# Kernel tuning notes

Hardware: AMD Instinct MI355X
Metric: run time of the kernel (lower is better)

Reference implementation:

```python
import jax, jax.numpy as jnp
import numpy as np

EPS = 1e-05
NEG = -1000000000.0

def rmsnorm(x):
    var = jnp.mean(x * x, axis=-1, keepdims=True)
    return x * jax.lax.rsqrt(var + EPS)

def apply_rotary(x, cos, sin):
    # x: [B,T,H,D], cos/sin: [T,D]
    d = x.shape[-1]
    x1, x2 = x[..., : d // 2], x[..., d // 2 :]
    half_rot = jnp.concatenate([-x2, x1], axis=-1)
    c = cos[None, :, None, :]
    s = sin[None, :, None, :]
    return x * c + half_rot * s

def setup_inputs() -> dict:
    key = jax.random.key(0)
    ks = jax.random.split(key, 12)
    B, T, C, H = 2, 2048, 1024, 16
    hd = C // H
    std = 0.02
    return {
        "x": jax.random.normal(ks[0], (B, T, C), jnp.float32),
        "x0": jax.random.normal(ks[1], (B, T, C), jnp.float32),
        "lambdaResid": jnp.ones((), jnp.float32),
        "lambdaX0": jnp.ones((), jnp.float32),
        "cos": jax.random.uniform(ks[2], (T, hd), jnp.float32),
        "sin": jax.random.uniform(ks[3], (T, hd), jnp.float32),
        "qWeight": jax.random.normal(ks[4], (C, C), jnp.float32) * std,
        "kWeight": jax.random.normal(ks[5], (C, C), jnp.float32) * std,
        "vWeight": jax.random.normal(ks[6], (C, C), jnp.float32) * std,
        "projWeight": jax.random.normal(ks[7], (C, C), jnp.float32) * std,
        "fcWeight": jax.random.normal(ks[8], (C, 4 * C), jnp.float32) * std,
        "mlpProjWeight": jax.random.normal(ks[9], (4 * C, C), jnp.float32) * std,
    }

def reference(x, x0, lambdaResid, lambdaX0, cos, sin,
              qWeight, kWeight, vWeight, projWeight, fcWeight, mlpProjWeight):
    B, T, C = x.shape
    hd = cos.shape[-1]
    H = C // hd
    scaled = x * lambdaResid + x0 * lambdaX0
    pre = rmsnorm(scaled)
    q = (pre @ qWeight).reshape(B, T, H, hd)
    k = (pre @ kWeight).reshape(B, T, H, hd)
    v = (pre @ vWeight).reshape(B, T, H, hd)
    q = rmsnorm(apply_rotary(q, cos, sin))  # [B,T,H,D]
    k = rmsnorm(apply_rotary(k, cos, sin))
    scores = jnp.einsum('bthd,bshd->bhts', q, k) / jnp.sqrt(jnp.float32(hd))
    mask = jnp.tril(jnp.ones((T, T), bool))
    scores = jnp.where(mask[None, None], scores, NEG)
    probs = jax.nn.softmax(scores, axis=-1)
    attn = jnp.einsum('bhts,bshd->bthd', probs, v).reshape(B, T, C)
    scaled = scaled + attn @ projWeight
    h = rmsnorm(scaled) @ fcWeight
    h = jnp.square(jax.nn.relu(h))
    return scaled + h @ mlpProjWeight
```

## Files before the change

kernel.cpp:

```cpp
#include <hip/hip_runtime.h>
#include <hip/hip_bf16.h>
#include <stdint.h>

typedef _Float16 f16;
typedef __attribute__((ext_vector_type(8))) _Float16 f16x8;
typedef __attribute__((ext_vector_type(4))) _Float16 f16x4;
typedef __attribute__((ext_vector_type(4))) float f32x4;

__device__ __forceinline__ void g2l16(const void* g, void* l) {
  __builtin_amdgcn_global_load_lds(
      (const __attribute__((address_space(1))) uint32_t*)g,
      (__attribute__((address_space(3))) uint32_t*)l, 16, 0, 0);
}

__global__ __launch_bounds__(256)
void wconv_all_kernel(const float* __restrict__ Wq, const float* __restrict__ Wk,
                      const float* __restrict__ Wv, const float* __restrict__ Wp,
                      const float* __restrict__ Wfc, const float* __restrict__ Wmp,
                      f16* __restrict__ Dq, f16* __restrict__ Dk, f16* __restrict__ Dv,
                      f16* __restrict__ Dp, f16* __restrict__ Dfc, f16* __restrict__ Dmp)
{
  __shared__ float tile[32][33];
  int id = blockIdx.x;
  const float* W; f16* Wt; int K, N, local;
  if      (id < 1024) { W = Wq;  Wt = Dq;  K = 1024; N = 1024; local = id; }
  else if (id < 2048) { W = Wk;  Wt = Dk;  K = 1024; N = 1024; local = id - 1024; }
  else if (id < 3072) { W = Wv;  Wt = Dv;  K = 1024; N = 1024; local = id - 2048; }
  else if (id < 4096) { W = Wp;  Wt = Dp;  K = 1024; N = 1024; local = id - 3072; }
  else if (id < 8192) { W = Wfc; Wt = Dfc; K = 1024; N = 4096; local = id - 4096; }
  else                { W = Wmp; Wt = Dmp; K = 4096; N = 1024; local = id - 8192; }
  int ntx = N >> 5;
  int n0 = (local % ntx) * 32, k0 = (local / ntx) * 32;
  int tx = threadIdx.x & 31, ty = threadIdx.x >> 5;
#pragma unroll
  for (int i = 0; i < 4; ++i)
    tile[ty + 8*i][tx] = W[(size_t)(k0 + ty + 8*i) * N + (n0 + tx)];
  __syncthreads();
#pragma unroll
  for (int i = 0; i < 4; ++i)
    Wt[(size_t)(n0 + ty + 8*i) * K + (k0 + tx)] = (f16)tile[tx][ty + 8*i];
}

__global__ __launch_bounds__(256)
void scale_rms_kernel(const float* __restrict__ x, const float* __restrict__ x0,
                      const float* __restrict__ lamR, const float* __restrict__ lamX,
                      float* __restrict__ scaled, f16* __restrict__ pre)
{
  const int C = 1024;
  int row = blockIdx.x, tid = threadIdx.x;
  float lr = lamR[0], lx = lamX[0];
  size_t base = (size_t)row * C;
  float4 xv = ((const float4*)(x + base))[tid];
  float4 zv = ((const float4*)(x0 + base))[tid];
  float4 sv;
  sv.x = xv.x*lr + zv.x*lx;  sv.y = xv.y*lr + zv.y*lx;
  sv.z = xv.z*lr + zv.z*lx;  sv.w = xv.w*lr + zv.w*lx;
  float ss = sv.x*sv.x + sv.y*sv.y + sv.z*sv.z + sv.w*sv.w;
#pragma unroll
  for (int off = 32; off >= 1; off >>= 1) ss += __shfl_xor(ss, off);
  __shared__ float red[4];
  if ((tid & 63) == 0) red[tid >> 6] = ss;
  __syncthreads();
  float tot = red[0] + red[1] + red[2] + red[3];
  float rs = rsqrtf(tot * (1.0f / 1024.0f) + 1e-5f);
  ((float4*)(scaled + base))[tid] = sv;
  f16* p = pre + base + tid * 4;
  p[0] = (f16)(sv.x * rs); p[1] = (f16)(sv.y * rs);
  p[2] = (f16)(sv.z * rs); p[3] = (f16)(sv.w * rs);
}

__global__ __launch_bounds__(256)
void combine_rms_kernel(const float* __restrict__ resid, const f16* __restrict__ p0,
                        const f16* __restrict__ p1, float* __restrict__ scaled2,
                        f16* __restrict__ pre2)
{
  const int C = 1024;
  int row = blockIdx.x, tid = threadIdx.x;
  size_t base = (size_t)row * C;
  float4 rv = ((const float4*)(resid + base))[tid];
  f16x4 av = ((const f16x4*)(p0 + base))[tid];
  f16x4 bv = ((const f16x4*)(p1 + base))[tid];
  float4 sv;
  sv.x = rv.x + (float)av[0] + (float)bv[0];
  sv.y = rv.y + (float)av[1] + (float)bv[1];
  sv.z = rv.z + (float)av[2] + (float)bv[2];
  sv.w = rv.w + (float)av[3] + (float)bv[3];
  float ss = sv.x*sv.x + sv.y*sv.y + sv.z*sv.z + sv.w*sv.w;
#pragma unroll
  for (int off = 32; off >= 1; off >>= 1) ss += __shfl_xor(ss, off);
  __shared__ float red[4];
  if ((tid & 63) == 0) red[tid >> 6] = ss;
  __syncthreads();
  float tot = red[0] + red[1] + red[2] + red[3];
  float rs = rsqrtf(tot * (1.0f / 1024.0f) + 1e-5f);
  ((float4*)(scaled2 + base))[tid] = sv;
  f16* p = pre2 + base + tid * 4;
  p[0] = (f16)(sv.x * rs); p[1] = (f16)(sv.y * rs);
  p[2] = (f16)(sv.z * rs); p[3] = (f16)(sv.w * rs);
}

__global__ __launch_bounds__(256)
void combine_out4_kernel(const float* __restrict__ resid, const f16* __restrict__ parts,
                         size_t pstride, float* __restrict__ out)
{
  size_t i = (size_t)blockIdx.x * 256 + threadIdx.x;
  float4 rv = ((const float4*)resid)[i];
  float4 sv = rv;
#pragma unroll
  for (int z = 0; z < 4; ++z) {
    f16x4 av = ((const f16x4*)(parts + z * pstride))[i];
    sv.x += (float)av[0]; sv.y += (float)av[1];
    sv.z += (float)av[2]; sv.w += (float)av[3];
  }
  ((float4*)out)[i] = sv;
}

__global__ __launch_bounds__(256)
void rope_rms_kernel(f16* __restrict__ Xq, f16* __restrict__ Xk,
                     const float* __restrict__ cs, const float* __restrict__ sn)
{
  const int MH = 4096 * 16;
  int ridx = blockIdx.x * 4 + (threadIdx.x >> 6);
  f16* X = (ridx < MH) ? Xq : Xk;
  if (ridx >= MH) ridx -= MH;
  int lane = threadIdx.x & 63;
  int h = ridx & 15;
  int bt = ridx >> 4;
  int t = bt & 2047;
  size_t base = (size_t)bt * 1024 + h * 64;
  float xv = (float)X[base + lane];
  float other = __shfl_xor(xv, 32);
  float rot = (lane < 32) ? -other : other;
  float c = cs[t * 64 + lane], s = sn[t * 64 + lane];
  float y = xv * c + rot * s;
  float ss = y * y;
#pragma unroll
  for (int off = 32; off >= 1; off >>= 1) ss += __shfl_xor(ss, off);
  float r = rsqrtf(ss * (1.0f / 64.0f) + 1e-5f);
  X[base + lane] = (f16)(y * r);
}

template<int EPI>
__global__ __launch_bounds__(256)
void gemm_kernel(const f16* __restrict__ A, const f16* __restrict__ Bt,
                 void* __restrict__ out, int M, int N, int K, int nb, int zb)
{
  __shared__ __align__(16) f16 smem[4 * 128 * 32];
  const int tid = threadIdx.x;
  const int wave = tid >> 6, lane = tid & 63;
  const int col = lane & 15, quad = lane >> 4;
  const int id = blockIdx.x;
  const int xcd = id & 7, s = id >> 3;
  const int n_i = s % nb;
  const int p = s / nb;
  const int mpx = (M >> 7) >> 3;
  const int zz = p / mpx;
  const int m_i = xcd * mpx + (p % mpx);
  const int m0 = m_i * 128, n0 = n_i * 128;
  const int wm = (wave >> 1) * 64, wn = (wave & 1) * 64;
  const int Ksub = K / zb;
  const int kBeg = zz * Ksub;
  const int nIter = Ksub >> 5;
  f32x4 acc[4][4] = {};

  const size_t rowb = (size_t)K * 2;
  const char* Agp = (const char*)A  + (size_t)m0 * rowb;
  const char* Bgp = (const char*)Bt + (size_t)n0 * rowb;

  const int r_st = (tid >> 2);
  const int cb_st = (tid & 3) << 4;
  const int lb0 = (wave * 64) << 4;
  const int lb1 = (256 + wave * 64) << 4;

#define STAGE(buf, k0)                                                           \
  {                                                                              \
    const size_t koff = (size_t)(k0) * 2;                                        \
    g2l16(Agp + (size_t)r_st * rowb + koff + cb_st,                              \
          (char*)smem + (buf) * 8192 + lb0);                                     \
    g2l16(Agp + (size_t)(r_st + 64) * rowb + koff + cb_st,                       \
          (char*)smem + (buf) * 8192 + lb1);                                     \
    g2l16(Bgp + (size_t)r_st * rowb + koff + cb_st,                              \
          (char*)smem + 16384 + (buf) * 8192 + lb0);                             \
    g2l16(Bgp + (size_t)(r_st + 64) * rowb + koff + cb_st,                       \
          (char*)smem + 16384 + (buf) * 8192 + lb1);                             \
  }

  STAGE(0, kBeg)
  for (int kt = 0; kt < nIter; ++kt) {
    __syncthreads();
    if (kt + 1 < nIter) STAGE((kt + 1) & 1, kBeg + (kt + 1) * 32)
    const f16* As = smem + (kt & 1) * 4096;
    const f16* Bs = smem + 8192 + (kt & 1) * 4096;
    f16x8 af[4], bf[4];
#pragma unroll
    for (int t = 0; t < 4; ++t)
      af[t] = *(const f16x8*)(As + (wm + t*16 + col) * 32 + quad * 8);
#pragma unroll
    for (int t = 0; t < 4; ++t)
      bf[t] = *(const f16x8*)(Bs + (wn + t*16 + col) * 32 + quad * 8);
#pragma unroll
    for (int mt = 0; mt < 4; ++mt)
#pragma unroll
      for (int nt = 0; nt < 4; ++nt)
        acc[mt][nt] = __builtin_amdgcn_mfma_f32_16x16x32_f16(af[mt], bf[nt], acc[mt][nt], 0, 0, 0);
  }
#undef STAGE
  f16* ep = smem + wave * 1024;
  f16* outz = (EPI == 4) ? ((f16*)out + (size_t)zz * M * N) : (f16*)out;
#pragma unroll
  for (int mt = 0; mt < 4; ++mt) {
#pragma unroll
    for (int nt = 0; nt < 4; ++nt) {
#pragma unroll
      for (int r = 0; r < 4; ++r) {
        float v = acc[mt][nt][r];
        if (EPI == 1) { float tv = v > 0.0f ? v : 0.0f; v = tv * tv; }
        ep[(quad * 4 + r) * 64 + ((nt ^ quad) * 16 + col)] = (f16)v;
      }
    }
#pragma unroll
    for (int j = 0; j < 2; ++j) {
      int e = j * 64 + lane;
      int row = e >> 3, rb = e & 7;
      int phys16 = (((rb >> 1) ^ (row >> 2)) << 1) + (rb & 1);
      f16x8 vv = *(const f16x8*)(ep + row * 64 + phys16 * 8);
      int grow = m0 + wm + mt * 16 + row;
      int gcol = n0 + wn + rb * 8;
      *(f16x8*)(outz + (size_t)grow * N + gcol) = vv;
    }
  }
}


__device__ __forceinline__ void stage256(const char* Agp, const char* Bgp, size_t rowb,
                                         char* lds, int st_r, size_t koff, int tid)
{
#pragma unroll
  for (int j = 0; j < 4; ++j) {
    g2l16(Agp + (size_t)(st_r + j * 64) * rowb + koff, lds + j * 8192 + tid * 16);
    g2l16(Bgp + (size_t)(st_r + j * 64) * rowb + koff, lds + 32768 + j * 8192 + tid * 16);
  }
}

template<int EPI>
__global__ __launch_bounds__(512, 2)
void gemm256_kernel(const f16* __restrict__ A, const f16* __restrict__ Bt,
                    void* __restrict__ out, int M, int N, int K, int nb, int zb)
{
  __shared__ __align__(16) f16 smem[65536];
  const int tid = threadIdx.x;
  const int wave = tid >> 6, lane = tid & 63;
  const int col = lane & 15, quad = lane >> 4;
  const int id = blockIdx.x;
  const int xcd = id & 7, sb = id >> 3;
  const int n_i = sb % nb;
  const int p = sb / nb;
  const int mpx = (M >> 8) >> 3;
  const int zz = p / mpx;
  const int m_i = xcd * mpx + (p % mpx);
  const int m0 = m_i * 256, n0 = n_i * 256;
  const int wm = (wave >> 2) * 128, wn = (wave & 3) * 64;
  const int Ksub = K / zb;
  const int kBeg = zz * Ksub;
  const int ntiles = Ksub >> 6;
  f32x4 acc[8][4] = {};

  const size_t rowb = (size_t)K * 2;
  const char* Agp = (const char*)A  + (size_t)m0 * rowb;
  const char* Bgp = (const char*)Bt + (size_t)n0 * rowb;

  const int st_r = tid >> 3;
  const size_t st_so = (size_t)(((tid & 7) ^ ((tid >> 3) & 7)) << 4);

  stage256(Agp, Bgp, rowb, (char*)smem,         st_r, (size_t)kBeg * 2 + st_so, tid);
  stage256(Agp, Bgp, rowb, (char*)smem + 65536, st_r, (size_t)(kBeg + 64) * 2 + st_so, tid);

  for (int t = 0; t < ntiles; ++t) {
    if (t < ntiles - 1) asm volatile("s_waitcnt vmcnt(8)" ::: "memory");
    else                asm volatile("s_waitcnt vmcnt(0)" ::: "memory");
    __builtin_amdgcn_s_barrier();
    asm volatile("" ::: "memory");

    const f16* As = smem + (t & 1) * 32768;
    const f16* Bs = As + 16384;
    f16x8 bf[4][2];
#pragma unroll
    for (int ct = 0; ct < 4; ++ct)
#pragma unroll
      for (int ks = 0; ks < 2; ++ks)
        bf[ct][ks] = *(const f16x8*)(Bs + (wn + ct*16 + col) * 64 +
                                     (((ks*4 + quad) ^ (col & 7)) << 3));
#pragma unroll
    for (int sp = 0; sp < 4; ++sp) {
      f16x8 af[2][2];
#pragma unroll
      for (int i = 0; i < 2; ++i)
#pragma unroll
        for (int ks = 0; ks < 2; ++ks)
          af[i][ks] = *(const f16x8*)(As + (wm + (sp*2 + i)*16 + col) * 64 +
                                      (((ks*4 + quad) ^ (col & 7)) << 3));
      __builtin_amdgcn_s_setprio(1);
#pragma unroll
      for (int i = 0; i < 2; ++i)
#pragma unroll
        for (int ct = 0; ct < 4; ++ct)
#pragma unroll
          for (int ks = 0; ks < 2; ++ks)
            acc[sp*2 + i][ct] = __builtin_amdgcn_mfma_f32_16x16x32_f16(
                af[i][ks], bf[ct][ks], acc[sp*2 + i][ct], 0, 0, 0);
      __builtin_amdgcn_s_setprio(0);
    }

    asm volatile("s_waitcnt lgkmcnt(0)" ::: "memory");
    __builtin_amdgcn_s_barrier();
    asm volatile("" ::: "memory");
    if (t + 2 < ntiles)
      stage256(Agp, Bgp, rowb, (char*)smem + (t & 1) * 65536, st_r,
               (size_t)(kBeg + (t + 2) * 64) * 2 + st_so, tid);
  }

  f16* ep = smem + wave * 1024;
  f16* outz = (EPI == 4) ? ((f16*)out + (size_t)zz * M * N) : (f16*)out;
#pragma unroll
  for (int mt = 0; mt < 8; ++mt) {
#pragma unroll
    for (int ct = 0; ct < 4; ++ct) {
#pragma unroll
      for (int r = 0; r < 4; ++r) {
        float v = acc[mt][ct][r];
        if (EPI == 1) { float tv = v > 0.0f ? v : 0.0f; v = tv * tv; }
        ep[(quad * 4 + r) * 64 + ((ct ^ quad) * 16 + col)] = (f16)v;
      }
    }
#pragma unroll
    for (int j = 0; j < 2; ++j) {
      int e = j * 64 + lane;
      int row = e >> 3, rb = e & 7;
      int phys16 = (((rb >> 1) ^ (row >> 2)) << 1) + (rb & 1);
      f16x8 vv = *(const f16x8*)(ep + row * 64 + phys16 * 8);
      int grow = m0 + wm + mt * 16 + row;
      int gcol = n0 + wn + rb * 8;
      *(f16x8*)(outz + (size_t)grow * N + gcol) = vv;
    }
  }
}

__global__ __launch_bounds__(512, 2)
void gemm256_qkv_kernel(const f16* __restrict__ A, const f16* __restrict__ Bt,
                        f16* __restrict__ qb, f16* __restrict__ kbuf, f16* __restrict__ vtg)
{
  const int K = 1024, nb = 12, ntiles = 16;
  __shared__ __align__(16) f16 smem[65536];
  const int tid = threadIdx.x;
  const int wave = tid >> 6, lane = tid & 63;
  const int col = lane & 15, quad = lane >> 4;
  const int id = blockIdx.x;
  const int xcd = id & 7, sb = id >> 3;
  const int n_i = sb % nb;
  const int m_i = xcd * 2 + (sb / nb);
  const int m0 = m_i * 256, n0 = n_i * 256;
  const int wm = (wave >> 2) * 128, wn = (wave & 3) * 64;
  f32x4 acc[8][4] = {};

  const size_t rowb = (size_t)K * 2;
  const char* Agp = (const char*)A  + (size_t)m0 * rowb;
  const char* Bgp = (const char*)Bt + (size_t)n0 * rowb;

  const int st_r = tid >> 3;
  const size_t st_so = (size_t)(((tid & 7) ^ ((tid >> 3) & 7)) << 4);

  stage256(Agp, Bgp, rowb, (char*)smem,         st_r, st_so, tid);
  stage256(Agp, Bgp, rowb, (char*)smem + 65536, st_r, (size_t)64 * 2 + st_so, tid);

  for (int t = 0; t < ntiles; ++t) {
    if (t < ntiles - 1) asm volatile("s_waitcnt vmcnt(8)" ::: "memory");
    else                asm volatile("s_waitcnt vmcnt(0)" ::: "memory");
    __builtin_amdgcn_s_barrier();
    asm volatile("" ::: "memory");

    const f16* As = smem + (t & 1) * 32768;
    const f16* Bs = As + 16384;
    f16x8 bf[4][2];
#pragma unroll
    for (int ct = 0; ct < 4; ++ct)
#pragma unroll
      for (int ks = 0; ks < 2; ++ks)
        bf[ct][ks] = *(const f16x8*)(Bs + (wn + ct*16 + col) * 64 +
                                     (((ks*4 + quad) ^ (col & 7)) << 3));
#pragma unroll
    for (int sp = 0; sp < 4; ++sp) {
      f16x8 af[2][2];
#pragma unroll
      for (int i = 0; i < 2; ++i)
#pragma unroll
        for (int ks = 0; ks < 2; ++ks)
          af[i][ks] = *(const f16x8*)(As + (wm + (sp*2 + i)*16 + col) * 64 +
                                      (((ks*4 + quad) ^ (col & 7)) << 3));
      __builtin_amdgcn_s_setprio(1);
#pragma unroll
      for (int i = 0; i < 2; ++i)
#pragma unroll
        for (int ct = 0; ct < 4; ++ct)
#pragma unroll
          for (int ks = 0; ks < 2; ++ks)
            acc[sp*2 + i][ct] = __builtin_amdgcn_mfma_f32_16x16x32_f16(
                af[i][ks], bf[ct][ks], acc[sp*2 + i][ct], 0, 0, 0);
      __builtin_amdgcn_s_setprio(0);
    }

    asm volatile("s_waitcnt lgkmcnt(0)" ::: "memory");
    __builtin_amdgcn_s_barrier();
    asm volatile("" ::: "memory");
    if (t + 2 < ntiles)
      stage256(Agp, Bgp, rowb, (char*)smem + (t & 1) * 65536, st_r,
               (size_t)((t + 2) * 64) * 2 + st_so, tid);
  }

  const int cw = n0 + wn;
  const int sel = cw >> 10;
  if (sel < 2) {
    f16* dst = (sel == 0) ? qb : kbuf;
    const int cbase = cw & 1023;
    f16* ep = smem + wave * 1024;
#pragma unroll
    for (int mt = 0; mt < 8; ++mt) {
#pragma unroll
      for (int ct = 0; ct < 4; ++ct)
#pragma unroll
        for (int r = 0; r < 4; ++r)
          ep[(quad * 4 + r) * 64 + ((ct ^ quad) * 16 + col)] = (f16)acc[mt][ct][r];
#pragma unroll
      for (int j = 0; j < 2; ++j) {
        int e = j * 64 + lane;
        int row = e >> 3, rb = e & 7;
        int phys16 = (((rb >> 1) ^ (row >> 2)) << 1) + (rb & 1);
        f16x8 vv = *(const f16x8*)(ep + row * 64 + phys16 * 8);
        int grow = m0 + wm + mt * 16 + row;
        *(f16x8*)(dst + (size_t)grow * 1024 + cbase + rb * 8) = vv;
      }
    }
  } else {
#pragma unroll
    for (int mt = 0; mt < 8; ++mt) {
      int t0 = m0 + wm + mt * 16 + quad * 4;
      int b = t0 >> 11, t = t0 & 2047;
#pragma unroll
      for (int ct = 0; ct < 4; ++ct) {
        int dd = (cw & 1023) + ct * 16 + col;
        int hh = dd >> 6, d = dd & 63;
        f16x4 vv;
#pragma unroll
        for (int r = 0; r < 4; ++r) vv[r] = (f16)acc[mt][ct][r];
        *(f16x4*)(vtg + ((size_t)((b * 16 + hh) * 64 + d)) * 2048 + t) = vv;
      }
    }
  }
}

__global__ __launch_bounds__(256)
void attn_kernel(const f16* __restrict__ Q, const f16* __restrict__ Kc,
                 const f16* __restrict__ Vt, f16* __restrict__ O)
{
  const int T = 2048, C = 1024;
  __shared__ __align__(16) f16 Ks[2][64 * 64];
  __shared__ __align__(16) f16 Vs[2][64 * 64];
  __shared__ __align__(16) f16 Ps[4][16 * 64];
  const int tid = threadIdx.x, wave = tid >> 6, lane = tid & 63;
  const int col = lane & 15, quad = lane >> 4;
  const int bh = blockIdx.x, b = bh >> 4, h = bh & 15;
  const int qt = (int)gridDim.y - 1 - (int)blockIdx.y;
  const int q0 = qt * 64;

  const f16* qb = Q  + ((size_t)b * T) * C + h * 64;
  const f16* kb = Kc + ((size_t)b * T) * C + h * 64;
  const f16* vb = Vt + ((size_t)bh * 64) * T;

  f16x8 aq[2];
#pragma unroll
  for (int ks = 0; ks < 2; ++ks)
    aq[ks] = *(const f16x8*)(qb + (size_t)(q0 + wave*16 + col) * C + ks*32 + quad*8);

  f32x4 o_acc[4];
#pragma unroll
  for (int dt = 0; dt < 4; ++dt) o_acc[dt] = (f32x4){0.f,0.f,0.f,0.f};
  float l_part[4] = {0.f, 0.f, 0.f, 0.f};

  const int srow = lane >> 3;
  const int sblk = (lane & 7) ^ srow;

#pragma unroll
  for (int i = 0; i < 2; ++i) {
    int r0 = wave * 16 + 8 * i;
    g2l16(kb + (size_t)(r0 + srow) * C + sblk * 8, (char*)Ks[0] + r0 * 128);
    g2l16(vb + (size_t)(r0 + srow) * T + sblk * 8, (char*)Vs[0] + r0 * 128);
  }

  int cur = 0;
  for (int kt = 0; kt <= qt; ++kt) {
    __syncthreads();

    if (kt < qt) {
      const int ks1 = (kt + 1) * 64;
#pragma unroll
      for (int i = 0; i < 2; ++i) {
        int r0 = wave * 16 + 8 * i;
        g2l16(kb + (size_t)(ks1 + r0 + srow) * C + sblk * 8, (char*)Ks[cur ^ 1] + r0 * 128);
        g2l16(vb + (size_t)(r0 + srow) * T + ks1 + sblk * 8, (char*)Vs[cur ^ 1] + r0 * 128);
      }
    }

    f32x4 s[4];
#pragma unroll
    for (int nt = 0; nt < 4; ++nt) s[nt] = (f32x4){0.f,0.f,0.f,0.f};
#pragma unroll
    for (int ks = 0; ks < 2; ++ks) {
#pragma unroll
      for (int nt = 0; nt < 4; ++nt) {
        int key = nt * 16 + col;
        f16x8 bk = *(const f16x8*)(Ks[cur] + key * 64 + (((ks*4 + quad) ^ (key & 7)) * 8));
        s[nt] = __builtin_amdgcn_mfma_f32_16x16x32_f16(aq[ks], bk, s[nt], 0, 0, 0);
      }
    }

    const bool masked = (kt == qt);
#pragma unroll
    for (int r = 0; r < 4; ++r) {
      const int qloc = quad * 4 + r;
      float p[4];
#pragma unroll
      for (int nt = 0; nt < 4; ++nt) {
        float pv = __expf(s[nt][r] * 0.125f);
        if (masked && (nt * 16 + col > wave * 16 + qloc)) pv = 0.0f;
        p[nt] = pv;
      }
      l_part[r] += (p[0] + p[1]) + (p[2] + p[3]);
#pragma unroll
      for (int nt = 0; nt < 4; ++nt) {
        int kblk = nt * 2 + (col >> 3);
        Ps[wave][qloc * 64 + ((kblk ^ (qloc & 7)) * 8) + (col & 7)] = (f16)p[nt];
      }
    }

#pragma unroll
    for (int ks = 0; ks < 2; ++ks) {
      f16x8 ap = *(const f16x8*)(&Ps[wave][0] + col * 64 + (((ks*4 + quad) ^ (col & 7)) * 8));
#pragma unroll
      for (int dt = 0; dt < 4; ++dt) {
        int d = dt * 16 + col;
        f16x8 bv = *(const f16x8*)(Vs[cur] + d * 64 + (((ks*4 + quad) ^ (d & 7)) * 8));
        o_acc[dt] = __builtin_amdgcn_mfma_f32_16x16x32_f16(ap, bv, o_acc[dt], 0, 0, 0);
      }
    }
    cur ^= 1;
  }

#pragma unroll
  for (int r = 0; r < 4; ++r) {
#pragma unroll
    for (int off = 8; off >= 1; off >>= 1)
      l_part[r] += __shfl_xor(l_part[r], off, 16);
  }
#pragma unroll
  for (int dt = 0; dt < 4; ++dt) {
#pragma unroll
    for (int r = 0; r < 4; ++r) {
      int qr = q0 + wave * 16 + quad * 4 + r;
      float v = o_acc[dt][r] / l_part[r];
      O[((size_t)b * T + qr) * C + h * 64 + dt * 16 + col] = (f16)v;
    }
  }
}

extern "C" void kernel_launch(void* const* d_in, const int* in_sizes, int n_in,
                              void* d_out, int out_size, void* d_ws, size_t ws_size,
                              hipStream_t stream)
{
  const float* x    = (const float*)d_in[0];
  const float* x0   = (const float*)d_in[1];
  const float* lamR = (const float*)d_in[2];
  const float* lamX = (const float*)d_in[3];
  const float* cs   = (const float*)d_in[4];
  const float* sn   = (const float*)d_in[5];
  const float* Wq   = (const float*)d_in[6];
  const float* Wk   = (const float*)d_in[7];
  const float* Wv   = (const float*)d_in[8];
  const float* Wp   = (const float*)d_in[9];
  const float* Wfc  = (const float*)d_in[10];
  const float* Wmp  = (const float*)d_in[11];
  float* out = (float*)d_out;

  const int B = 2, T = 2048, C = 1024, H = 16;
  const int M = B * T;
  const size_t MB = 1ull << 20;
  char* ws = (char*)d_ws;
  f16*   Wqkv_t = (f16*)(ws + 0 * MB);
  f16*   Wp_t   = (f16*)(ws + 6 * MB);
  f16*   Wfc_t  = (f16*)(ws + 8 * MB);
  f16*   Wmp_t  = (f16*)(ws + 16 * MB);
  float* scaled  = (float*)(ws + 24 * MB);
  f16*   pre     = (f16*)(ws + 40 * MB);
  f16*   qb      = (f16*)(ws + 48 * MB);
  f16*   kbuf    = (f16*)(ws + 56 * MB);
  f16*   vtg     = (f16*)(ws + 64 * MB);
  float* scaled2 = (float*)(ws + 72 * MB);
  f16*   hbuf    = (f16*)(ws + 88 * MB);
  f16*   attnOut = pre;
  f16*   pre2    = qb;
  f16*   projP   = (f16*)(ws + 88 * MB);
  f16*   mlpP    = (f16*)(ws + 24 * MB);

  dim3 tb(256);
  dim3 tb5(512);
  wconv_all_kernel<<<dim3(12288), tb, 0, stream>>>(
      Wq, Wk, Wv, Wp, Wfc, Wmp,
      Wqkv_t, Wqkv_t + 1024*1024, Wqkv_t + 2048*1024, Wp_t, Wfc_t, Wmp_t);

  scale_rms_kernel<<<M, tb, 0, stream>>>(x, x0, lamR, lamX, scaled, pre);

  gemm256_qkv_kernel<<<dim3(192), tb5, 0, stream>>>(pre, Wqkv_t, qb, kbuf, vtg);

  rope_rms_kernel<<<(M * H) / 2, tb, 0, stream>>>(qb, kbuf, cs, sn);

  attn_kernel<<<dim3(B * H, T/64), tb, 0, stream>>>(qb, kbuf, vtg, attnOut);

  gemm_kernel<4><<<dim3(8 * 32 * 2), tb, 0, stream>>>(attnOut, Wp_t, projP, M, C, C, 8, 2);
  combine_rms_kernel<<<M, tb, 0, stream>>>(scaled, projP, projP + (size_t)M*C, scaled2, pre2);

  gemm256_kernel<1><<<dim3(256), tb5, 0, stream>>>(pre2, Wfc_t, hbuf, M, 4*C, C, 16, 1);

  gemm256_kernel<4><<<dim3(256), tb5, 0, stream>>>(hbuf, Wmp_t, mlpP, M, C, 4*C, 4, 4);
  combine_out4_kernel<<<(M*C)/1024, tb, 0, stream>>>(scaled2, mlpP, (size_t)M*C, out);
}
```

Baseline: 349.8 us.

## Pair causal query tiles per attention block to balance work and share K/V loads

The attention kernel now launches 512-thread blocks, each handling two query tiles: a high tile (31-pr) with one four-wave group and a low tile (pr) with the other. The two groups share the double-buffered K/V tiles in LDS, so each key tile is loaded once for both. Pairing tiles this way gives every block the same amount of causal work and halves the grid. The low-tile waves go idle once they pass their diagonal but still hit the barriers, and the larger block may reduce occupancy.

New measurement: 347.6 us. No clear change (-0.6%).

```diff
diff --git a/kernel.cpp b/kernel.cpp
--- a/kernel.cpp
+++ b/kernel.cpp
@@ -231,7 +231,6 @@
   }
 }
 
-
 __device__ __forceinline__ void stage256(const char* Agp, const char* Bgp, size_t rowb,
                                          char* lds, int st_r, size_t koff, int tid)
 {
@@ -457,19 +456,23 @@
   }
 }
 
-__global__ __launch_bounds__(256)
+__global__ __launch_bounds__(512)
 void attn_kernel(const f16* __restrict__ Q, const f16* __restrict__ Kc,
                  const f16* __restrict__ Vt, f16* __restrict__ O)
 {
   const int T = 2048, C = 1024;
   __shared__ __align__(16) f16 Ks[2][64 * 64];
   __shared__ __align__(16) f16 Vs[2][64 * 64];
-  __shared__ __align__(16) f16 Ps[4][16 * 64];
+  __shared__ __align__(16) f16 Ps[8][16 * 64];
   const int tid = threadIdx.x, wave = tid >> 6, lane = tid & 63;
   const int col = lane & 15, quad = lane >> 4;
   const int bh = blockIdx.x, b = bh >> 4, h = bh & 15;
-  const int qt = (int)gridDim.y - 1 - (int)blockIdx.y;
-  const int q0 = qt * 64;
+  const int pr = blockIdx.y;
+  const int grp = wave >> 2;
+  const int w4 = wave & 3;
+  const int hiB = 31 - pr;
+  const int myB = grp ? pr : hiB;
+  const int q0 = myB * 64;
 
   const f16* qb = Q  + ((size_t)b * T) * C + h * 64;
   const f16* kb = Kc + ((size_t)b * T) * C + h * 64;
@@ -478,7 +481,7 @@
   f16x8 aq[2];
 #pragma unroll
   for (int ks = 0; ks < 2; ++ks)
-    aq[ks] = *(const f16x8*)(qb + (size_t)(q0 + wave*16 + col) * C + ks*32 + quad*8);
+    aq[ks] = *(const f16x8*)(qb + (size_t)(q0 + w4*16 + col) * C + ks*32 + quad*8);
 
   f32x4 o_acc[4];
 #pragma unroll
@@ -487,68 +490,63 @@
 
   const int srow = lane >> 3;
   const int sblk = (lane & 7) ^ srow;
-
-#pragma unroll
-  for (int i = 0; i < 2; ++i) {
-    int r0 = wave * 16 + 8 * i;
-    g2l16(kb + (size_t)(r0 + srow) * C + sblk * 8, (char*)Ks[0] + r0 * 128);
-    g2l16(vb + (size_t)(r0 + srow) * T + sblk * 8, (char*)Vs[0] + r0 * 128);
-  }
+  const int r0 = wave * 8;
+
+  g2l16(kb + (size_t)(r0 + srow) * C + sblk * 8, (char*)Ks[0] + r0 * 128);
+  g2l16(vb + (size_t)(r0 + srow) * T + sblk * 8, (char*)Vs[0] + r0 * 128);
 
   int cur = 0;
-  for (int kt = 0; kt <= qt; ++kt) {
+  for (int kt = 0; kt <= hiB; ++kt) {
     __syncthreads();
 
-    if (kt < qt) {
+    if (kt < hiB) {
       const int ks1 = (kt + 1) * 64;
-#pragma unroll
-      for (int i = 0; i < 2; ++i) {
-        int r0 = wave * 16 + 8 * i;
-        g2l16(kb + (size_t)(ks1 + r0 + srow) * C + sblk * 8, (char*)Ks[cur ^ 1] + r0 * 128);
-        g2l16(vb + (size_t)(r0 + srow) * T + ks1 + sblk * 8, (char*)Vs[cur ^ 1] + r0 * 128);
+      g2l16(kb + (size_t)(ks1 + r0 + srow) * C + sblk * 8, (char*)Ks[cur ^ 1] + r0 * 128);
+      g2l16(vb + (size_t)(r0 + srow) * T + ks1 + sblk * 8, (char*)Vs[cur ^ 1] + r0 * 128);
+    }
+
+    if (kt <= myB) {
+      f32x4 s[4];
+#pragma unroll
+      for (int nt = 0; nt < 4; ++nt) s[nt] = (f32x4){0.f,0.f,0.f,0.f};
+#pragma unroll
+      for (int ks = 0; ks < 2; ++ks) {
+#pragma unroll
+        for (int nt = 0; nt < 4; ++nt) {
+          int key = nt * 16 + col;
+          f16x8 bk = *(const f16x8*)(Ks[cur] + key * 64 + (((ks*4 + quad) ^ (key & 7)) * 8));
+          s[nt] = __builtin_amdgcn_mfma_f32_16x16x32_f16(aq[ks], bk, s[nt], 0, 0, 0);
+        }
       }
-    }
-
-    f32x4 s[4];
-#pragma unroll
-    for (int nt = 0; nt < 4; ++nt) s[nt] = (f32x4){0.f,0.f,0.f,0.f};
-#pragma unroll
-    for (int ks = 0; ks < 2; ++ks) {
-#pragma unroll
-      for (int nt = 0; nt < 4; ++nt) {
-        int key = nt * 16 + col;
-        f16x8 bk = *(const f16x8*)(Ks[cur] + key * 64 + (((ks*4 + quad) ^ (key & 7)) * 8));
-        s[nt] = __builtin_amdgcn_mfma_f32_16x16x32_f16(aq[ks], bk, s[nt], 0, 0, 0);
+
+      const bool masked = (kt == myB);
+#pragma unroll
+      for (int r = 0; r < 4; ++r) {
+        const int qloc = quad * 4 + r;
+        float p[4];
+#pragma unroll
+        for (int nt = 0; nt < 4; ++nt) {
+          float pv = __expf(s[nt][r] * 0.125f);
+          if (masked && (nt * 16 + col > w4 * 16 + qloc)) pv = 0.0f;
+          p[nt] = pv;
+        }
+        l_part[r] += (p[0] + p[1]) + (p[2] + p[3]);
+#pragma unroll
+        for (int nt = 0; nt < 4; ++nt) {
+          int kblk = nt * 2 + (col >> 3);
+          Ps[wave][qloc * 64 + ((kblk ^ (qloc & 7)) * 8) + (col & 7)] = (f16)p[nt];
+        }
       }
-    }
-
-    const bool masked = (kt == qt);
-#pragma unroll
-    for (int r = 0; r < 4; ++r) {
-      const int qloc = quad * 4 + r;
-      float p[4];
-#pragma unroll
-      for (int nt = 0; nt < 4; ++nt) {
-        float pv = __expf(s[nt][r] * 0.125f);
-        if (masked && (nt * 16 + col > wave * 16 + qloc)) pv = 0.0f;
-        p[nt] = pv;
-      }
-      l_part[r] += (p[0] + p[1]) + (p[2] + p[3]);
-#pragma unroll
-      for (int nt = 0; nt < 4; ++nt) {
-        int kblk = nt * 2 + (col >> 3);
-        Ps[wave][qloc * 64 + ((kblk ^ (qloc & 7)) * 8) + (col & 7)] = (f16)p[nt];
-      }
-    }
-
-#pragma unroll
-    for (int ks = 0; ks < 2; ++ks) {
-      f16x8 ap = *(const f16x8*)(&Ps[wave][0] + col * 64 + (((ks*4 + quad) ^ (col & 7)) * 8));
-#pragma unroll
-      for (int dt = 0; dt < 4; ++dt) {
-        int d = dt * 16 + col;
-        f16x8 bv = *(const f16x8*)(Vs[cur] + d * 64 + (((ks*4 + quad) ^ (d & 7)) * 8));
-        o_acc[dt] = __builtin_amdgcn_mfma_f32_16x16x32_f16(ap, bv, o_acc[dt], 0, 0, 0);
+
+#pragma unroll
+      for (int ks = 0; ks < 2; ++ks) {
+        f16x8 ap = *(const f16x8*)(&Ps[wave][0] + col * 64 + (((ks*4 + quad) ^ (col & 7)) * 8));
+#pragma unroll
+        for (int dt = 0; dt < 4; ++dt) {
+          int d = dt * 16 + col;
+          f16x8 bv = *(const f16x8*)(Vs[cur] + d * 64 + (((ks*4 + quad) ^ (d & 7)) * 8));
+          o_acc[dt] = __builtin_amdgcn_mfma_f32_16x16x32_f16(ap, bv, o_acc[dt], 0, 0, 0);
+        }
       }
     }
     cur ^= 1;
@@ -564,7 +562,7 @@
   for (int dt = 0; dt < 4; ++dt) {
 #pragma unroll
     for (int r = 0; r < 4; ++r) {
-      int qr = q0 + wave * 16 + quad * 4 + r;
+      int qr = q0 + w4 * 16 + quad * 4 + r;
       float v = o_acc[dt][r] / l_part[r];
       O[((size_t)b * T + qr) * C + h * 64 + dt * 16 + col] = (f16)v;
     }
@@ -621,7 +619,7 @@
 
   rope_rms_kernel<<<(M * H) / 2, tb, 0, stream>>>(qb, kbuf, cs, sn);
 
-  attn_kernel<<<dim3(B * H, T/64), tb, 0, stream>>>(qb, kbuf, vtg, attnOut);
+  attn_kernel<<<dim3(B * H, 16), tb5, 0, stream>>>(qb, kbuf, vtg, attnOut);
 
   gemm_kernel<4><<<dim3(8 * 32 * 2), tb, 0, stream>>>(attnOut, Wp_t, projP, M, C, C, 8, 2);
   combine_rms_kernel<<<M, tb, 0, stream>>>(scaled, projP, projP + (size_t)M*C, scaled2, pre2);
```

## Keep attention probabilities in registers by transposing QK^T MFMA operands

Applied to the files above, without the earlier changes.

Swaps the MFMA operand order for QK^T so each lane holds scores for one query across keys. The probabilities are then packed to fp16 with cvt_pkrtz and rearranged with cross-lane shuffles to form the A operand of the PV MFMA, removing the per-wave LDS scratch round trip. It also adds s_setprio around the MFMA sections, raises the occupancy hint to 5 waves per SIMD, and replaces the final division with a reciprocal multiply. The cost is extra shuffles, split V reads, and round-toward-zero fp16 conversion of the probabilities.

New measurement: 349.7 us. No clear change (-0.0%).

```diff
diff --git a/kernel.cpp b/kernel.cpp
--- a/kernel.cpp
+++ b/kernel.cpp
@@ -5,12 +5,19 @@
 typedef _Float16 f16;
 typedef __attribute__((ext_vector_type(8))) _Float16 f16x8;
 typedef __attribute__((ext_vector_type(4))) _Float16 f16x4;
+typedef __attribute__((ext_vector_type(2))) __fp16 fp16x2;
 typedef __attribute__((ext_vector_type(4))) float f32x4;
 
 __device__ __forceinline__ void g2l16(const void* g, void* l) {
   __builtin_amdgcn_global_load_lds(
       (const __attribute__((address_space(1))) uint32_t*)g,
       (__attribute__((address_space(3))) uint32_t*)l, 16, 0, 0);
+}
+
+__device__ __forceinline__ uint32_t pkrtz(float a, float b) {
+  union { fp16x2 h; uint32_t u; } z;
+  z.h = __builtin_amdgcn_cvt_pkrtz(a, b);
+  return z.u;
 }
 
 __global__ __launch_bounds__(256)
@@ -231,7 +238,6 @@
   }
 }
 
-
 __device__ __forceinline__ void stage256(const char* Agp, const char* Bgp, size_t rowb,
                                          char* lds, int st_r, size_t koff, int tid)
 {
@@ -457,14 +463,13 @@
   }
 }
 
-__global__ __launch_bounds__(256)
+__global__ __launch_bounds__(256, 5)
 void attn_kernel(const f16* __restrict__ Q, const f16* __restrict__ Kc,
                  const f16* __restrict__ Vt, f16* __restrict__ O)
 {
   const int T = 2048, C = 1024;
   __shared__ __align__(16) f16 Ks[2][64 * 64];
   __shared__ __align__(16) f16 Vs[2][64 * 64];
-  __shared__ __align__(16) f16 Ps[4][16 * 64];
   const int tid = threadIdx.x, wave = tid >> 6, lane = tid & 63;
   const int col = lane & 15, quad = lane >> 4;
   const int bh = blockIdx.x, b = bh >> 4, h = bh & 15;
@@ -475,15 +480,15 @@
   const f16* kb = Kc + ((size_t)b * T) * C + h * 64;
   const f16* vb = Vt + ((size_t)bh * 64) * T;
 
-  f16x8 aq[2];
+  f16x8 bq[2];
 #pragma unroll
   for (int ks = 0; ks < 2; ++ks)
-    aq[ks] = *(const f16x8*)(qb + (size_t)(q0 + wave*16 + col) * C + ks*32 + quad*8);
+    bq[ks] = *(const f16x8*)(qb + (size_t)(q0 + wave*16 + col) * C + ks*32 + quad*8);
 
   f32x4 o_acc[4];
 #pragma unroll
   for (int dt = 0; dt < 4; ++dt) o_acc[dt] = (f32x4){0.f,0.f,0.f,0.f};
-  float l_part[4] = {0.f, 0.f, 0.f, 0.f};
+  float l_acc = 0.f;
 
   const int srow = lane >> 3;
   const int sblk = (lane & 7) ^ srow;
@@ -494,6 +499,14 @@
     g2l16(kb + (size_t)(r0 + srow) * C + sblk * 8, (char*)Ks[0] + r0 * 128);
     g2l16(vb + (size_t)(r0 + srow) * T + sblk * 8, (char*)Vs[0] + r0 * 128);
   }
+
+  const int cm = col & 7;
+  const int c00 = quad,            c01 = 4 + (quad ^ 1);
+  const int c10 = 8 + (quad ^ 2),  c11 = 12 + (quad ^ 3);
+  const int o00 = (((c00 >> 1) ^ cm) << 3) + ((c00 & 1) << 2);
+  const int o01 = (((c01 >> 1) ^ cm) << 3) + ((c01 & 1) << 2);
+  const int o10 = (((c10 >> 1) ^ cm) << 3) + ((c10 & 1) << 2);
+  const int o11 = (((c11 >> 1) ^ cm) << 3) + ((c11 & 1) << 2);
 
   int cur = 0;
   for (int kt = 0; kt <= qt; ++kt) {
@@ -512,60 +525,76 @@
     f32x4 s[4];
 #pragma unroll
     for (int nt = 0; nt < 4; ++nt) s[nt] = (f32x4){0.f,0.f,0.f,0.f};
+    __builtin_amdgcn_s_setprio(1);
 #pragma unroll
     for (int ks = 0; ks < 2; ++ks) {
 #pragma unroll
       for (int nt = 0; nt < 4; ++nt) {
         int key = nt * 16 + col;
-        f16x8 bk = *(const f16x8*)(Ks[cur] + key * 64 + (((ks*4 + quad) ^ (key & 7)) * 8));
-        s[nt] = __builtin_amdgcn_mfma_f32_16x16x32_f16(aq[ks], bk, s[nt], 0, 0, 0);
+        f16x8 ak = *(const f16x8*)(Ks[cur] + key * 64 + (((ks*4 + quad) ^ (key & 7)) * 8));
+        s[nt] = __builtin_amdgcn_mfma_f32_16x16x32_f16(ak, bq[ks], s[nt], 0, 0, 0);
       }
     }
+    __builtin_amdgcn_s_setprio(0);
 
     const bool masked = (kt == qt);
-#pragma unroll
-    for (int r = 0; r < 4; ++r) {
-      const int qloc = quad * 4 + r;
+    const int qloc = wave * 16 + col;
+    uint32_t pk[4][2];
+    float l_tile = 0.f;
+#pragma unroll
+    for (int nt = 0; nt < 4; ++nt) {
       float p[4];
 #pragma unroll
-      for (int nt = 0; nt < 4; ++nt) {
+      for (int r = 0; r < 4; ++r) {
         float pv = __expf(s[nt][r] * 0.125f);
-        if (masked && (nt * 16 + col > wave * 16 + qloc)) pv = 0.0f;
-        p[nt] = pv;
+        if (masked && (nt * 16 + quad * 4 + r > qloc)) pv = 0.0f;
+        p[r] = pv;
       }
-      l_part[r] += (p[0] + p[1]) + (p[2] + p[3]);
-#pragma unroll
-      for (int nt = 0; nt < 4; ++nt) {
-        int kblk = nt * 2 + (col >> 3);
-        Ps[wave][qloc * 64 + ((kblk ^ (qloc & 7)) * 8) + (col & 7)] = (f16)p[nt];
-      }
-    }
-
-#pragma unroll
-    for (int ks = 0; ks < 2; ++ks) {
-      f16x8 ap = *(const f16x8*)(&Ps[wave][0] + col * 64 + (((ks*4 + quad) ^ (col & 7)) * 8));
-#pragma unroll
-      for (int dt = 0; dt < 4; ++dt) {
-        int d = dt * 16 + col;
-        f16x8 bv = *(const f16x8*)(Vs[cur] + d * 64 + (((ks*4 + quad) ^ (d & 7)) * 8));
-        o_acc[dt] = __builtin_amdgcn_mfma_f32_16x16x32_f16(ap, bv, o_acc[dt], 0, 0, 0);
-      }
-    }
+      l_tile += (p[0] + p[1]) + (p[2] + p[3]);
+      pk[nt][0] = pkrtz(p[0], p[1]);
+      pk[nt][1] = pkrtz(p[2], p[3]);
+    }
+    l_acc += l_tile;
+
+    union { uint32_t u[4]; f16x8 v; } pa0, pa1;
+    pa0.u[0] = pk[0][0];
+    pa0.u[1] = pk[0][1];
+    pa0.u[2] = (uint32_t)__shfl_xor((int)pk[1][0], 16);
+    pa0.u[3] = (uint32_t)__shfl_xor((int)pk[1][1], 16);
+    pa1.u[0] = (uint32_t)__shfl_xor((int)pk[2][0], 32);
+    pa1.u[1] = (uint32_t)__shfl_xor((int)pk[2][1], 32);
+    pa1.u[2] = (uint32_t)__shfl_xor((int)pk[3][0], 48);
+    pa1.u[3] = (uint32_t)__shfl_xor((int)pk[3][1], 48);
+
+    __builtin_amdgcn_s_setprio(1);
+#pragma unroll
+    for (int dt = 0; dt < 4; ++dt) {
+      const f16* vrow = Vs[cur] + (dt * 16 + col) * 64;
+      union { struct { f16x4 lo, hi; } p; f16x8 v; } bv0, bv1;
+      bv0.p.lo = *(const f16x4*)(vrow + o00);
+      bv0.p.hi = *(const f16x4*)(vrow + o01);
+      bv1.p.lo = *(const f16x4*)(vrow + o10);
+      bv1.p.hi = *(const f16x4*)(vrow + o11);
+      o_acc[dt] = __builtin_amdgcn_mfma_f32_16x16x32_f16(pa0.v, bv0.v, o_acc[dt], 0, 0, 0);
+      o_acc[dt] = __builtin_amdgcn_mfma_f32_16x16x32_f16(pa1.v, bv1.v, o_acc[dt], 0, 0, 0);
+    }
+    __builtin_amdgcn_s_setprio(0);
     cur ^= 1;
   }
 
-#pragma unroll
-  for (int r = 0; r < 4; ++r) {
-#pragma unroll
-    for (int off = 8; off >= 1; off >>= 1)
-      l_part[r] += __shfl_xor(l_part[r], off, 16);
-  }
+  l_acc += __shfl_xor(l_acc, 16);
+  l_acc += __shfl_xor(l_acc, 32);
+  float linv[4];
+#pragma unroll
+  for (int r = 0; r < 4; ++r)
+    linv[r] = 1.0f / __shfl(l_acc, quad * 4 + r);
+
 #pragma unroll
   for (int dt = 0; dt < 4; ++dt) {
 #pragma unroll
     for (int r = 0; r < 4; ++r) {
       int qr = q0 + wave * 16 + quad * 4 + r;
-      float v = o_acc[dt][r] / l_part[r];
+      float v = o_acc[dt][r] * linv[r];
       O[((size_t)b * T + qr) * C + h * 64 + dt * 16 + col] = (f16)v;
     }
   }
```
